# Kernel tuning notes

Hardware: AMD Instinct MI355X
Metric: run time of the kernel (lower is better)

Reference implementation:

```python
import jax, jax.numpy as jnp
import numpy as np

HEADS = 8

def setup_inputs() -> dict:
    key = jax.random.key(0)
    ks = jax.random.split(key, 10)
    B, S, E = 2, 2048, 512
    q = jax.random.normal(ks[0], (B, S, E), jnp.float32)
    k = jax.random.normal(ks[1], (B, S, E), jnp.float32)
    v = jax.random.normal(ks[2], (B, S, E), jnp.float32)
    mask = jnp.zeros((S, S), jnp.float32)  # additive mask [s_q, s_k]
    scale = 0.02
    Wq = jax.random.normal(ks[3], (E, E), jnp.float32) * scale
    bq = jax.random.normal(ks[4], (E,), jnp.float32) * scale
    Wk = jax.random.normal(ks[5], (E, E), jnp.float32) * scale
    bk = jax.random.normal(ks[6], (E,), jnp.float32) * scale
    Wv = jax.random.normal(ks[7], (E, E), jnp.float32) * scale
    bv = jax.random.normal(ks[8], (E,), jnp.float32) * scale
    return {"q": q, "k": k, "v": v, "mask": mask,
            "Wq": Wq, "bq": bq, "Wk": Wk, "bk": bk, "Wv": Wv, "bv": bv}

def reference(q, k, v, mask, Wq, bq, Wk, bk, Wv, bv):
    H = HEADS
    b, s_q, _ = q.shape
    s_k = k.shape[1]
    s_v = v.shape[1]
    # NOTE: faithful to source: row-major view(b, H, s, -1) WITHOUT transposing
    # seq/head axes first (quirk of the original module).
    K = jnp.swapaxes((k @ Wk.T + bk).reshape(b, H, s_k, -1), 2, 3)  # [b,H,dh,s_k]
    Q = (q @ Wq.T + bq).reshape(b, H, s_q, -1)                      # [b,H,s_q,dh]
    V = (v @ Wv.T + bv).reshape(b, H, s_v, -1)                      # [b,H,s_v,dh]
    # NOTE: original scales by sqrt(K.shape[-1]) AFTER the transpose, i.e. sqrt(s_k)
    scores = (Q @ K) / jnp.sqrt(jnp.asarray(s_k, jnp.float32))      # [b,H,s_q,s_k]
    scores = scores + mask[:s_q, :s_k]
    attn = jax.nn.softmax(scores, axis=-1)
    out = (attn @ V).reshape(b, s_q, -1)  # [b, s_q, e]
    return out
```

## Files before the change

kernel.cpp:

```cpp
#include <hip/hip_runtime.h>


#define SEQ 2048
#define EMB 512
#define DH  64
#define MROWS 4096
#define NROWS 32768

typedef float  v4f __attribute__((ext_vector_type(4)));
typedef short  v8s __attribute__((ext_vector_type(8)));
typedef __fp16 v2h __attribute__((ext_vector_type(2)));

static __device__ __forceinline__ unsigned int f2bf(float f) {
    unsigned int u = __float_as_uint(f);
    u += 0x7fffu + ((u >> 16) & 1u);
    return u >> 16;
}
static __device__ __forceinline__ unsigned int pack2(float a, float b) {
    return f2bf(a) | (f2bf(b) << 16);
}
static __device__ __forceinline__ unsigned int packh2(float a, float b) {
    v2h h = __builtin_amdgcn_cvt_pkrtz(a, b);
    return __builtin_bit_cast(unsigned int, h);
}

__global__ __launch_bounds__(256, 3) void proj_kernel(
    const float* __restrict__ q, const float* __restrict__ k, const float* __restrict__ v,
    const float* __restrict__ Wq, const float* __restrict__ bq,
    const float* __restrict__ Wk, const float* __restrict__ bk,
    const float* __restrict__ Wv, const float* __restrict__ bv,
    unsigned short* __restrict__ Qbf, unsigned short* __restrict__ Kbf,
    unsigned short* __restrict__ Vbf)
{
    __shared__ __align__(16) char smem[27648];
    char* As = smem;
    char* Ws = smem + 9216;

    const int id  = blockIdx.x;
    const int pos = id & 31;
    const int nb  = pos >> 3;
    const int unit = (id >> 5) * 8 + (pos & 7);
    const int mb = unit & 63;
    const int z  = unit >> 6;

    const float* A    = (z == 0) ? q  : (z == 1) ? k  : v;
    const float* W    = (z == 0) ? Wq : (z == 1) ? Wk : Wv;
    const float* bias = (z == 0) ? bq : (z == 1) ? bk : bv;
    unsigned short* Cg = (z == 0) ? Qbf : (z == 1) ? Kbf : Vbf;

    const int tid  = threadIdx.x;
    const int w    = tid >> 6;
    const int lane = tid & 63;
    const int qd   = lane >> 4;
    const int n    = lane & 15;
    const int m0 = mb * 64, n0 = nb * 128;

    float4 areg[4], wreg[8];
#pragma unroll
    for (int i = 0; i < 4; ++i) {
        int c = tid + i * 256;
        areg[i] = *(const float4*)&A[(size_t)(m0 + (c >> 4)) * EMB + (c & 15) * 4];
    }
#pragma unroll
    for (int i = 0; i < 8; ++i) {
        int c = tid + i * 256;
        wreg[i] = *(const float4*)&W[(size_t)(n0 + (c >> 4)) * EMB + (c & 15) * 4];
    }

    v4f acc[8];
#pragma unroll
    for (int cb = 0; cb < 8; ++cb) acc[cb] = (v4f)0.f;

#pragma unroll 1
    for (int kt = 0; kt < 8; ++kt) {
        __syncthreads();
#pragma unroll
        for (int i = 0; i < 4; ++i) {
            int c = tid + i * 256;
            uint2 pk = { pack2(areg[i].x, areg[i].y), pack2(areg[i].z, areg[i].w) };
            *(uint2*)&As[(c >> 4) * 144 + (c & 15) * 8] = pk;
        }
#pragma unroll
        for (int i = 0; i < 8; ++i) {
            int c = tid + i * 256;
            uint2 pk = { pack2(wreg[i].x, wreg[i].y), pack2(wreg[i].z, wreg[i].w) };
            *(uint2*)&Ws[(c >> 4) * 144 + (c & 15) * 8] = pk;
        }
        __syncthreads();

        if (kt + 1 < 8) {
#pragma unroll
            for (int i = 0; i < 4; ++i) {
                int c = tid + i * 256;
                areg[i] = *(const float4*)&A[(size_t)(m0 + (c >> 4)) * EMB + (kt+1) * 64 + (c & 15) * 4];
            }
#pragma unroll
            for (int i = 0; i < 8; ++i) {
                int c = tid + i * 256;
                wreg[i] = *(const float4*)&W[(size_t)(n0 + (c >> 4)) * EMB + (kt+1) * 64 + (c & 15) * 4];
            }
        }

#pragma unroll
        for (int ks = 0; ks < 2; ++ks) {
            v8s af = *(const v8s*)&As[(w * 16 + n) * 144 + ks * 64 + qd * 16];
#pragma unroll
            for (int cb = 0; cb < 8; ++cb) {
                v8s bfr = *(const v8s*)&Ws[(cb * 16 + n) * 144 + ks * 64 + qd * 16];
                acc[cb] = __builtin_amdgcn_mfma_f32_16x16x32_bf16(af, bfr, acc[cb], 0, 0, 0);
            }
        }
    }

    float bb[8];
#pragma unroll
    for (int cb = 0; cb < 8; ++cb) bb[cb] = bias[n0 + cb * 16 + n];
#pragma unroll
    for (int cb = 0; cb < 8; ++cb)
#pragma unroll
        for (int r = 0; r < 4; ++r) acc[cb][r] += bb[cb];

    __syncthreads();
    short* Ct = (short*)smem;
#pragma unroll
    for (int cb = 0; cb < 8; ++cb)
#pragma unroll
        for (int r = 0; r < 4; ++r)
            Ct[(w * 16 + qd * 4 + r) * 136 + cb * 16 + n] = (short)f2bf(acc[cb][r]);
    __syncthreads();
    const int rr = tid >> 2, q4 = tid & 3;
#pragma unroll
    for (int i = 0; i < 4; ++i) {
        uint4 t4 = *(const uint4*)&smem[rr * 272 + q4 * 64 + i * 16];
        *(uint4*)&Cg[(size_t)(m0 + rr) * EMB + n0 + q4 * 32 + i * 8] = t4;
    }
}

__global__ __launch_bounds__(256) void vtrans_kernel(
    const unsigned short* __restrict__ Vbf, unsigned short* __restrict__ VtT)
{
    __shared__ unsigned short T[64 * 136];
    const int bh = blockIdx.x, kt = blockIdx.y;
    const int tid = threadIdx.x;
    const unsigned short* Vh = Vbf + (size_t)bh * (SEQ * DH) + (size_t)kt * 64 * DH;
#pragma unroll
    for (int i = 0; i < 2; ++i) {
        int c = tid + i * 256;
        int s_l = c >> 3, ch = c & 7;
        uint4 t4 = *(const uint4*)&Vh[c * 8];
        const unsigned short* e = (const unsigned short*)&t4;
#pragma unroll
        for (int j = 0; j < 8; ++j)
            T[(ch * 8 + j) * 136 + s_l] = e[j];
    }
    __syncthreads();
    unsigned short* Ot = VtT + ((size_t)bh * 32 + kt) * (64 * 64);
    const int d = tid >> 2, sq = tid & 3;
#pragma unroll
    for (int i = 0; i < 2; ++i) {
        uint4 t4 = *(const uint4*)&T[d * 136 + sq * 16 + i * 8];
        *(uint4*)&Ot[d * 64 + sq * 16 + i * 8] = t4;
    }
}

__global__ __launch_bounds__(256) void maskt_kernel(
    const float* __restrict__ mask, unsigned int* __restrict__ maskT)
{
    const int rb = blockIdx.x, kt = blockIdx.y;
    const int tid = threadIdx.x;
    unsigned int* tile = maskT + ((size_t)rb * 32 + kt) * 4096;
#pragma unroll
    for (int i = 0; i < 8; ++i) {
        int s = tid + i * 256;
        int l  = s & 63;
        int cb = (s >> 6) & 3;
        int g  = (s >> 8) & 1;
        int w  = (s >> 9) & 3;
        int qd = l >> 4, n = l & 15;
        const float4 f = *(const float4*)&mask[
            (size_t)(rb * 128 + w * 32 + g * 16 + n) * SEQ + kt * 64 + cb * 16 + qd * 4];
        uint2 pk = { pack2(f.x, f.y), pack2(f.z, f.w) };
        *(uint2*)&tile[(size_t)s * 2] = pk;
    }
}

template <int SPLITS>
__global__ __launch_bounds__(256, 4) void attn_kernel(
    const unsigned short* __restrict__ Qbf, const unsigned short* __restrict__ Kbf,
    const unsigned short* __restrict__ VtT,
    const unsigned int* __restrict__ maskT, const float* __restrict__ maskf,
    unsigned short* __restrict__ Opart, float* __restrict__ ml,
    float* __restrict__ out)
{
    __shared__ __align__(16) char smem[36864];
    char* Ks  = smem;
    char* Vts = smem + 9216;

    const int tid  = threadIdx.x;
    const int w    = tid >> 6;
    const int lane = tid & 63;
    const int qd   = lane >> 4;
    const int n    = lane & 15;
    char* Ps = smem + 18432 + w * 4608;

    const int id = blockIdx.x;
    const int rb = ((id >> 3) & 1) * 8 + (id & 7);
    const int bh = (id >> 4) & 15;
    const int kq = id >> 8;
    const int KT0 = kq * (32 / SPLITS), KT1 = KT0 + 32 / SPLITS;

    const unsigned short* Qh = Qbf + (size_t)bh * (SEQ * DH);
    const unsigned short* Kh = Kbf + (size_t)bh * (SEQ * DH);
    const unsigned short* Vth = VtT + (size_t)bh * 32 * 4096;

    const float scale = 0.02209708691207961f;

    v8s qf[2][2];
#pragma unroll
    for (int g = 0; g < 2; ++g) {
        const size_t qrow = (size_t)(rb * 128 + w * 32 + g * 16 + n);
#pragma unroll
        for (int ks = 0; ks < 2; ++ks)
            qf[g][ks] = *(const v8s*)&Qh[qrow * DH + ks * 32 + qd * 8];
    }

    uint4 kreg[2], vreg[2];
#pragma unroll
    for (int p = 0; p < 2; ++p) {
        int c = tid + p * 256;
        kreg[p] = *(const uint4*)&Kh[(size_t)KT0 * 4096 + c * 8];
        vreg[p] = *(const uint4*)&Vth[(size_t)KT0 * 4096 + c * 8];
    }

    float m_[2] = { -1e30f, -1e30f }, l_[2] = { 0.f, 0.f };
    v4f oacc[2][4];
#pragma unroll
    for (int g = 0; g < 2; ++g)
#pragma unroll
        for (int cb = 0; cb < 4; ++cb) oacc[g][cb] = (v4f)0.f;

#pragma unroll 1
    for (int kt = KT0; kt < KT1; ++kt) {
        __syncthreads();
#pragma unroll
        for (int p = 0; p < 2; ++p) {
            int c = tid + p * 256;
            *(uint4*)&Ks [(c >> 3) * 144 + (c & 7) * 16] = kreg[p];
            *(uint4*)&Vts[(c >> 3) * 144 + (c & 7) * 16] = vreg[p];
        }
        __syncthreads();

        if (kt + 1 < KT1) {
#pragma unroll
            for (int p = 0; p < 2; ++p) {
                int c = tid + p * 256;
                kreg[p] = *(const uint4*)&Kh[(size_t)(kt + 1) * 4096 + c * 8];
                vreg[p] = *(const uint4*)&Vth[(size_t)(kt + 1) * 4096 + c * 8];
            }
        }

        uint2 mtu[2][4];
        float4 mk[2][4];
        if (SPLITS > 1) {
            const unsigned int* tile = maskT + ((size_t)rb * 32 + kt) * 4096;
#pragma unroll
            for (int g = 0; g < 2; ++g)
#pragma unroll
                for (int cb = 0; cb < 4; ++cb)
                    mtu[g][cb] = *(const uint2*)&tile[
                        (size_t)((((w * 2 + g) * 4 + cb) * 64) + qd * 16 + n) * 2];
        } else {
#pragma unroll
            for (int g = 0; g < 2; ++g) {
                const size_t mrow = (size_t)(rb * 128 + w * 32 + g * 16 + n);
#pragma unroll
                for (int cb = 0; cb < 4; ++cb)
                    mk[g][cb] = *(const float4*)&maskf[mrow * SEQ + kt * 64 + cb * 16 + qd * 4];
            }
        }

        v4f sacc[2][4];
#pragma unroll
        for (int g = 0; g < 2; ++g)
#pragma unroll
            for (int cb = 0; cb < 4; ++cb) sacc[g][cb] = (v4f)0.f;
#pragma unroll
        for (int ks = 0; ks < 2; ++ks)
#pragma unroll
            for (int cb = 0; cb < 4; ++cb) {
                v8s kf = *(const v8s*)&Ks[(cb * 16 + n) * 144 + ks * 64 + qd * 16];
#pragma unroll
                for (int g = 0; g < 2; ++g)
                    sacc[g][cb] = __builtin_amdgcn_mfma_f32_16x16x32_bf16(kf, qf[g][ks], sacc[g][cb], 0, 0, 0);
            }

#pragma unroll
        for (int g = 0; g < 2; ++g) {
            float sv[4][4];
            float mx = -1e30f;
#pragma unroll
            for (int cb = 0; cb < 4; ++cb) {
                float mv[4];
                if (SPLITS > 1) {
                    uint2 mu = mtu[g][cb];
                    mv[0] = __uint_as_float(mu.x << 16);
                    mv[1] = __uint_as_float(mu.x & 0xFFFF0000u);
                    mv[2] = __uint_as_float(mu.y << 16);
                    mv[3] = __uint_as_float(mu.y & 0xFFFF0000u);
                } else {
                    mv[0] = mk[g][cb].x; mv[1] = mk[g][cb].y;
                    mv[2] = mk[g][cb].z; mv[3] = mk[g][cb].w;
                }
#pragma unroll
                for (int r = 0; r < 4; ++r) {
                    float s = fmaf(sacc[g][cb][r], scale, mv[r]);
                    sv[cb][r] = s;
                    mx = fmaxf(mx, s);
                }
            }
            mx = fmaxf(mx, __shfl_xor(mx, 16));
            mx = fmaxf(mx, __shfl_xor(mx, 32));
            const float mnew  = fmaxf(m_[g], mx);
            const float alpha = __expf(m_[g] - mnew);
            float rs = 0.f;
            float pv[4][4];
#pragma unroll
            for (int cb = 0; cb < 4; ++cb)
#pragma unroll
                for (int r = 0; r < 4; ++r) {
                    float e = __expf(sv[cb][r] - mnew);
                    pv[cb][r] = e;
                    rs += e;
                }
            rs += __shfl_xor(rs, 16);
            rs += __shfl_xor(rs, 32);
            l_[g] = l_[g] * alpha + rs;
            m_[g] = mnew;
#pragma unroll
            for (int cb = 0; cb < 4; ++cb) {
#pragma unroll
                for (int r = 0; r < 4; ++r) oacc[g][cb][r] *= alpha;
                uint2 pk = { pack2(pv[cb][0], pv[cb][1]), pack2(pv[cb][2], pv[cb][3]) };
                *(uint2*)&Ps[(g * 16 + n) * 144 + cb * 32 + qd * 8] = pk;
            }
        }

#pragma unroll
        for (int ks = 0; ks < 2; ++ks) {
            v8s pf[2];
#pragma unroll
            for (int g = 0; g < 2; ++g)
                pf[g] = *(const v8s*)&Ps[(g * 16 + n) * 144 + ks * 64 + qd * 16];
#pragma unroll
            for (int cb = 0; cb < 4; ++cb) {
                v8s vf = *(const v8s*)&Vts[(cb * 16 + n) * 144 + ks * 64 + qd * 16];
#pragma unroll
                for (int g = 0; g < 2; ++g)
                    oacc[g][cb] = __builtin_amdgcn_mfma_f32_16x16x32_bf16(vf, pf[g], oacc[g][cb], 0, 0, 0);
            }
        }
    }

    if (SPLITS == 1) {
#pragma unroll
        for (int g = 0; g < 2; ++g) {
            const float inv = 1.0f / l_[g];
#pragma unroll
            for (int cb = 0; cb < 4; ++cb)
#pragma unroll
                for (int r = 0; r < 4; ++r) oacc[g][cb][r] *= inv;
        }
    } else {
        if (qd == 0) {
#pragma unroll
            for (int g = 0; g < 2; ++g) {
                const size_t row = (size_t)bh * SEQ + rb * 128 + w * 32 + g * 16 + n;
                ml[((size_t)kq * NROWS + row) * 2 + 0] = m_[g];
                ml[((size_t)kq * NROWS + row) * 2 + 1] = l_[g];
            }
        }
    }
    __syncthreads();
#pragma unroll
    for (int g = 0; g < 2; ++g)
#pragma unroll
        for (int cb = 0; cb < 4; ++cb)
            *(v4f*)&smem[(w * 32 + g * 16 + n) * 272 + cb * 64 + qd * 16] = oacc[g][cb];
    __syncthreads();
    const int r_l = tid >> 1, hf = tid & 1;
    if (SPLITS == 1) {
        float* dst = &out[((size_t)bh * SEQ + rb * 128 + r_l) * DH + hf * 32];
#pragma unroll
        for (int i = 0; i < 8; ++i) {
            float4 t4 = *(const float4*)&smem[r_l * 272 + hf * 128 + i * 16];
            *(float4*)&dst[i * 4] = t4;
        }
    } else {
        unsigned short* dst = &Opart[((size_t)kq * NROWS + (size_t)bh * SEQ + rb * 128 + r_l) * DH + hf * 32];
#pragma unroll
        for (int i = 0; i < 4; ++i) {
            float4 f0 = *(const float4*)&smem[r_l * 272 + hf * 128 + i * 32];
            float4 f1 = *(const float4*)&smem[r_l * 272 + hf * 128 + i * 32 + 16];
            uint4 o = { packh2(f0.x, f0.y), packh2(f0.z, f0.w),
                        packh2(f1.x, f1.y), packh2(f1.z, f1.w) };
            *(uint4*)&dst[i * 8] = o;
        }
    }
}

__global__ __launch_bounds__(256) void combine_kernel(
    const unsigned int* __restrict__ Opart, const float* __restrict__ ml,
    float* __restrict__ out, int splits)
{
    const int tid = threadIdx.x;
    const size_t row = (size_t)blockIdx.x * 16 + (tid >> 4);
    const int d4 = (tid & 15) * 4;
    float M = -1e30f;
    for (int s = 0; s < splits; ++s)
        M = fmaxf(M, ml[((size_t)s * NROWS + row) * 2]);
    float denom = 0.f;
    float4 o = make_float4(0.f, 0.f, 0.f, 0.f);
    for (int s = 0; s < splits; ++s) {
        const float ws = __expf(ml[((size_t)s * NROWS + row) * 2] - M);
        denom += ws * ml[((size_t)s * NROWS + row) * 2 + 1];
        uint2 u = *(const uint2*)&Opart[((size_t)s * NROWS + row) * 32 + (d4 >> 1)];
        v2h h0 = __builtin_bit_cast(v2h, u.x);
        v2h h1 = __builtin_bit_cast(v2h, u.y);
        o.x += ws * (float)h0.x; o.y += ws * (float)h0.y;
        o.z += ws * (float)h1.x; o.w += ws * (float)h1.y;
    }
    const float inv = 1.0f / denom;
    o.x *= inv; o.y *= inv; o.z *= inv; o.w *= inv;
    *(float4*)&out[row * DH + d4] = o;
}

extern "C" void kernel_launch(void* const* d_in, const int* in_sizes, int n_in,
                              void* d_out, int out_size, void* d_ws, size_t ws_size,
                              hipStream_t stream) {
    const float* q    = (const float*)d_in[0];
    const float* k    = (const float*)d_in[1];
    const float* v    = (const float*)d_in[2];
    const float* mask = (const float*)d_in[3];
    const float* Wq   = (const float*)d_in[4];
    const float* bq   = (const float*)d_in[5];
    const float* Wk   = (const float*)d_in[6];
    const float* bk   = (const float*)d_in[7];
    const float* Wv   = (const float*)d_in[8];
    const float* bv   = (const float*)d_in[9];

    char* ws = (char*)d_ws;
    const size_t MB = 1024 * 1024;
    unsigned short* Qbf   = (unsigned short*)(ws + 0);
    unsigned short* Kbf   = (unsigned short*)(ws + 4 * MB);
    unsigned short* VtT   = (unsigned short*)(ws + 8 * MB);
    unsigned short* Opart = (unsigned short*)(ws + 12 * MB);
    unsigned short* Vbf   = (unsigned short*)(ws + 12 * MB);
    float*          mlp   = (float*)(ws + 28 * MB);
    unsigned int*   maskT = (unsigned int*)(ws + 29 * MB);

    const size_t need_split = 37 * MB;
    const bool do_split = ws_size >= need_split;

    proj_kernel<<<768, 256, 0, stream>>>(q, k, v, Wq, bq, Wk, bk, Wv, bv,
                                         Qbf, Kbf, Vbf);

    dim3 tgrid(16, 32);
    vtrans_kernel<<<tgrid, 256, 0, stream>>>(Vbf, VtT);

    if (do_split) {
        dim3 mgrid(16, 32);
        maskt_kernel<<<mgrid, 256, 0, stream>>>(mask, maskT);
        attn_kernel<4><<<1024, 256, 0, stream>>>(Qbf, Kbf, VtT, maskT, mask,
                                                 Opart, mlp, (float*)d_out);
        combine_kernel<<<NROWS / 16, 256, 0, stream>>>((const unsigned int*)Opart,
                                                       mlp, (float*)d_out, 4);
    } else {
        attn_kernel<1><<<256, 256, 0, stream>>>(Qbf, Kbf, VtT, maskT, mask,
                                                Opart, mlp, (float*)d_out);
    }
}
```

Measured before the change: 188.0 us.

## Fold mask relayout into projection kernel and pre-scale Q

Result: faster. 182.9 us (-2.7%).

```diff
diff --git a/kernel.cpp b/kernel.cpp
--- a/kernel.cpp
+++ b/kernel.cpp
@@ -29,9 +29,31 @@
     const float* __restrict__ Wq, const float* __restrict__ bq,
     const float* __restrict__ Wk, const float* __restrict__ bk,
     const float* __restrict__ Wv, const float* __restrict__ bv,
+    const float* __restrict__ mask,
     unsigned short* __restrict__ Qbf, unsigned short* __restrict__ Kbf,
-    unsigned short* __restrict__ Vbf)
+    unsigned short* __restrict__ Vbf, float* __restrict__ maskT)
 {
+    const int tid = threadIdx.x;
+
+    if (blockIdx.x >= 768) {
+        const int mb2 = blockIdx.x - 768;
+        const int rb = mb2 >> 5, kt = mb2 & 31;
+        float* tile = maskT + ((size_t)rb * 32 + kt) * 8192;
+#pragma unroll
+        for (int i = 0; i < 8; ++i) {
+            int s = tid + i * 256;
+            int l  = s & 63;
+            int cb = (s >> 6) & 3;
+            int g  = (s >> 8) & 1;
+            int w  = (s >> 9) & 3;
+            int qd = l >> 4, n = l & 15;
+            float4 f = *(const float4*)&mask[
+                (size_t)(rb * 128 + w * 32 + g * 16 + n) * SEQ + kt * 64 + cb * 16 + qd * 4];
+            *(float4*)&tile[(size_t)s * 4] = f;
+        }
+        return;
+    }
+
     __shared__ __align__(16) char smem[27648];
     char* As = smem;
     char* Ws = smem + 9216;
@@ -48,7 +70,6 @@
     const float* bias = (z == 0) ? bq : (z == 1) ? bk : bv;
     unsigned short* Cg = (z == 0) ? Qbf : (z == 1) ? Kbf : Vbf;
 
-    const int tid  = threadIdx.x;
     const int w    = tid >> 6;
     const int lane = tid & 63;
     const int qd   = lane >> 4;
@@ -112,13 +133,14 @@
         }
     }
 
+    const float osc = (z == 0) ? 0.02209708691207961f : 1.0f;
     float bb[8];
 #pragma unroll
     for (int cb = 0; cb < 8; ++cb) bb[cb] = bias[n0 + cb * 16 + n];
 #pragma unroll
     for (int cb = 0; cb < 8; ++cb)
 #pragma unroll
-        for (int r = 0; r < 4; ++r) acc[cb][r] += bb[cb];
+        for (int r = 0; r < 4; ++r) acc[cb][r] = (acc[cb][r] + bb[cb]) * osc;
 
     __syncthreads();
     short* Ct = (short*)smem;
@@ -163,32 +185,11 @@
     }
 }
 
-__global__ __launch_bounds__(256) void maskt_kernel(
-    const float* __restrict__ mask, unsigned int* __restrict__ maskT)
-{
-    const int rb = blockIdx.x, kt = blockIdx.y;
-    const int tid = threadIdx.x;
-    unsigned int* tile = maskT + ((size_t)rb * 32 + kt) * 4096;
-#pragma unroll
-    for (int i = 0; i < 8; ++i) {
-        int s = tid + i * 256;
-        int l  = s & 63;
-        int cb = (s >> 6) & 3;
-        int g  = (s >> 8) & 1;
-        int w  = (s >> 9) & 3;
-        int qd = l >> 4, n = l & 15;
-        const float4 f = *(const float4*)&mask[
-            (size_t)(rb * 128 + w * 32 + g * 16 + n) * SEQ + kt * 64 + cb * 16 + qd * 4];
-        uint2 pk = { pack2(f.x, f.y), pack2(f.z, f.w) };
-        *(uint2*)&tile[(size_t)s * 2] = pk;
-    }
-}
-
 template <int SPLITS>
 __global__ __launch_bounds__(256, 4) void attn_kernel(
     const unsigned short* __restrict__ Qbf, const unsigned short* __restrict__ Kbf,
     const unsigned short* __restrict__ VtT,
-    const unsigned int* __restrict__ maskT, const float* __restrict__ maskf,
+    const float* __restrict__ maskT, const float* __restrict__ maskf,
     unsigned short* __restrict__ Opart, float* __restrict__ ml,
     float* __restrict__ out)
 {
@@ -213,8 +214,6 @@
     const unsigned short* Kh = Kbf + (size_t)bh * (SEQ * DH);
     const unsigned short* Vth = VtT + (size_t)bh * 32 * 4096;
 
-    const float scale = 0.02209708691207961f;
-
     v8s qf[2][2];
 #pragma unroll
     for (int g = 0; g < 2; ++g) {
@@ -250,6 +249,28 @@
         }
         __syncthreads();
 
+        v4f sacc[2][4];
+        float4 mk[2][4];
+        if (SPLITS > 1) {
+            const float* tileF = maskT + ((size_t)rb * 32 + kt) * 8192;
+#pragma unroll
+            for (int g = 0; g < 2; ++g)
+#pragma unroll
+                for (int cb = 0; cb < 4; ++cb)
+                    sacc[g][cb] = *(const v4f*)&tileF[
+                        (size_t)((((w * 2 + g) * 4 + cb) * 64) + qd * 16 + n) * 4];
+        } else {
+#pragma unroll
+            for (int g = 0; g < 2; ++g) {
+                const size_t mrow = (size_t)(rb * 128 + w * 32 + g * 16 + n);
+#pragma unroll
+                for (int cb = 0; cb < 4; ++cb) {
+                    mk[g][cb] = *(const float4*)&maskf[mrow * SEQ + kt * 64 + cb * 16 + qd * 4];
+                    sacc[g][cb] = (v4f)0.f;
+                }
+            }
+        }
+
         if (kt + 1 < KT1) {
 #pragma unroll
             for (int p = 0; p < 2; ++p) {
@@ -259,31 +280,6 @@
             }
         }
 
-        uint2 mtu[2][4];
-        float4 mk[2][4];
-        if (SPLITS > 1) {
-            const unsigned int* tile = maskT + ((size_t)rb * 32 + kt) * 4096;
-#pragma unroll
-            for (int g = 0; g < 2; ++g)
-#pragma unroll
-                for (int cb = 0; cb < 4; ++cb)
-                    mtu[g][cb] = *(const uint2*)&tile[
-                        (size_t)((((w * 2 + g) * 4 + cb) * 64) + qd * 16 + n) * 2];
-        } else {
-#pragma unroll
-            for (int g = 0; g < 2; ++g) {
-                const size_t mrow = (size_t)(rb * 128 + w * 32 + g * 16 + n);
-#pragma unroll
-                for (int cb = 0; cb < 4; ++cb)
-                    mk[g][cb] = *(const float4*)&maskf[mrow * SEQ + kt * 64 + cb * 16 + qd * 4];
-            }
-        }
-
-        v4f sacc[2][4];
-#pragma unroll
-        for (int g = 0; g < 2; ++g)
-#pragma unroll
-            for (int cb = 0; cb < 4; ++cb) sacc[g][cb] = (v4f)0.f;
 #pragma unroll
         for (int ks = 0; ks < 2; ++ks)
 #pragma unroll
@@ -296,27 +292,15 @@
 
 #pragma unroll
         for (int g = 0; g < 2; ++g) {
-            float sv[4][4];
             float mx = -1e30f;
 #pragma unroll
             for (int cb = 0; cb < 4; ++cb) {
-                float mv[4];
-                if (SPLITS > 1) {
-                    uint2 mu = mtu[g][cb];
-                    mv[0] = __uint_as_float(mu.x << 16);
-                    mv[1] = __uint_as_float(mu.x & 0xFFFF0000u);
-                    mv[2] = __uint_as_float(mu.y << 16);
-                    mv[3] = __uint_as_float(mu.y & 0xFFFF0000u);
-                } else {
-                    mv[0] = mk[g][cb].x; mv[1] = mk[g][cb].y;
-                    mv[2] = mk[g][cb].z; mv[3] = mk[g][cb].w;
+                if (SPLITS == 1) {
+                    sacc[g][cb][0] += mk[g][cb].x; sacc[g][cb][1] += mk[g][cb].y;
+                    sacc[g][cb][2] += mk[g][cb].z; sacc[g][cb][3] += mk[g][cb].w;
                 }
 #pragma unroll
-                for (int r = 0; r < 4; ++r) {
-                    float s = fmaf(sacc[g][cb][r], scale, mv[r]);
-                    sv[cb][r] = s;
-                    mx = fmaxf(mx, s);
-                }
+                for (int r = 0; r < 4; ++r) mx = fmaxf(mx, sacc[g][cb][r]);
             }
             mx = fmaxf(mx, __shfl_xor(mx, 16));
             mx = fmaxf(mx, __shfl_xor(mx, 32));
@@ -328,7 +312,7 @@
             for (int cb = 0; cb < 4; ++cb)
 #pragma unroll
                 for (int r = 0; r < 4; ++r) {
-                    float e = __expf(sv[cb][r] - mnew);
+                    float e = __expf(sacc[g][cb][r] - mnew);
                     pv[cb][r] = e;
                     rs += e;
                 }
@@ -456,25 +440,25 @@
     unsigned short* Opart = (unsigned short*)(ws + 12 * MB);
     unsigned short* Vbf   = (unsigned short*)(ws + 12 * MB);
     float*          mlp   = (float*)(ws + 28 * MB);
-    unsigned int*   maskT = (unsigned int*)(ws + 29 * MB);
-
-    const size_t need_split = 37 * MB;
+    float*          maskT = (float*)(ws + 29 * MB);
+
+    const size_t need_split = 45 * MB;
     const bool do_split = ws_size >= need_split;
 
-    proj_kernel<<<768, 256, 0, stream>>>(q, k, v, Wq, bq, Wk, bk, Wv, bv,
-                                         Qbf, Kbf, Vbf);
-
-    dim3 tgrid(16, 32);
-    vtrans_kernel<<<tgrid, 256, 0, stream>>>(Vbf, VtT);
-
     if (do_split) {
-        dim3 mgrid(16, 32);
-        maskt_kernel<<<mgrid, 256, 0, stream>>>(mask, maskT);
+        proj_kernel<<<1280, 256, 0, stream>>>(q, k, v, Wq, bq, Wk, bk, Wv, bv,
+                                              mask, Qbf, Kbf, Vbf, maskT);
+        dim3 tgrid(16, 32);
+        vtrans_kernel<<<tgrid, 256, 0, stream>>>(Vbf, VtT);
         attn_kernel<4><<<1024, 256, 0, stream>>>(Qbf, Kbf, VtT, maskT, mask,
                                                  Opart, mlp, (float*)d_out);
         combine_kernel<<<NROWS / 16, 256, 0, stream>>>((const unsigned int*)Opart,
                                                        mlp, (float*)d_out, 4);
     } else {
+        proj_kernel<<<768, 256, 0, stream>>>(q, k, v, Wq, bq, Wk, bk, Wv, bv,
+                                             mask, Qbf, Kbf, Vbf, maskT);
+        dim3 tgrid(16, 32);
+        vtrans_kernel<<<tgrid, 256, 0, stream>>>(Vbf, VtT);
         attn_kernel<1><<<256, 256, 0, stream>>>(Qbf, Kbf, VtT, maskT, mask,
                                                 Opart, mlp, (float*)d_out);
     }
```
